# Kernel tuning notes

Measured on AMD Instinct MI355X. Metric: run time of the kernel, lower is better.

The kernel has to match this reference:

```python
import jax, jax.numpy as jnp
import numpy as np

CHUNK = 2048   # chunk_size from __init__
EPS = 1e-5     # BatchNorm eps (torch default)


def _proj(x, w, gamma, beta, mean, var):
    # 1x1 conv (no bias) + BatchNorm (eval, running stats) + ReLU
    y = jnp.einsum('bchw,oc->bohw', x, w)
    scale = gamma / jnp.sqrt(var + EPS)
    y = (y - mean[None, :, None, None]) * scale[None, :, None, None] + beta[None, :, None, None]
    return jax.nn.relu(y)


def setup_inputs() -> dict:
    key = jax.random.key(0)
    ks = jax.random.split(key, 8)
    B, Cl, Ci, Co, H, W = 2, 256, 512, 128, 128, 128
    return {
        'lidar_features': jax.random.normal(ks[0], (B, Cl, H, W), jnp.float32),
        'image_features': jax.random.normal(ks[1], (B, Ci, H, W), jnp.float32),
        # kaiming_normal fan_out for 1x1 conv: std = sqrt(2 / Co)
        'lidar_w': jax.random.normal(ks[2], (Co, Cl), jnp.float32) * np.sqrt(2.0 / Co),
        'lidar_gamma': jnp.ones((Co,), jnp.float32),
        'lidar_beta': jnp.zeros((Co,), jnp.float32),
        'lidar_mean': jax.random.normal(ks[3], (Co,), jnp.float32) * 0.1,
        'lidar_var': jax.random.uniform(ks[4], (Co,), jnp.float32, 0.5, 1.5),
        'image_w': jax.random.normal(ks[5], (Co, Ci), jnp.float32) * np.sqrt(2.0 / Co),
        'image_gamma': jnp.ones((Co,), jnp.float32),
        'image_beta': jnp.zeros((Co,), jnp.float32),
        'image_mean': jax.random.normal(ks[6], (Co,), jnp.float32) * 0.1,
        'image_var': jax.random.uniform(ks[7], (Co,), jnp.float32, 0.5, 1.5),
        'modality_weights': jnp.ones((2,), jnp.float32),
    }


def reference(lidar_features, image_features,
              lidar_w, lidar_gamma, lidar_beta, lidar_mean, lidar_var,
              image_w, image_gamma, image_beta, image_mean, image_var,
              modality_weights):
    lidar_proj = _proj(lidar_features, lidar_w, lidar_gamma, lidar_beta, lidar_mean, lidar_var)
    image_proj = _proj(image_features, image_w, image_gamma, image_beta, image_mean, image_var)
    # spatial sizes match by construction, so no interpolation branch
    B, C, H, W = lidar_proj.shape
    P = H * W
    n = P // CHUNK  # P chosen divisible by CHUNK
    # block-diagonal attention: q from image, k=v from lidar, per pixel chunk
    q = image_proj.reshape(B, C, P).transpose(0, 2, 1).reshape(B, n, CHUNK, C)
    k = lidar_proj.reshape(B, C, P).transpose(0, 2, 1).reshape(B, n, CHUNK, C)
    attn = jax.nn.softmax(jnp.einsum('bnqc,bnkc->bnqk', q, k) / jnp.sqrt(jnp.float32(C)), axis=-1)
    out = jnp.einsum('bnqk,bnkc->bnqc', attn, k)  # v == k (both are lidar_proj)
    fused = out.reshape(B, P, C).transpose(0, 2, 1).reshape(B, C, H, W)
    w = jax.nn.softmax(modality_weights)
    return w[0] * image_proj + w[1] * fused
```

## Files before the change

### kernel.cpp

```cpp
#include <hip/hip_runtime.h>
#include <hip/hip_bf16.h>

typedef __attribute__((ext_vector_type(4))) float f32x4;
typedef __attribute__((ext_vector_type(8))) short short8;

#define P_TOT 16384
#define NCO 128
#define EPS 1e-5f
#define ALPHA 0.12752269f

__device__ __forceinline__ unsigned short f2bf(float f) {
  union { float f; unsigned u; } v; v.f = f;
  unsigned r = v.u + 0x7FFFu + ((v.u >> 16) & 1u);
  return (unsigned short)(r >> 16);
}
__device__ __forceinline__ float bf2f(unsigned short h) {
  union { unsigned u; float f; } v; v.u = ((unsigned)h) << 16;
  return v.f;
}
__device__ __forceinline__ unsigned cvtpk_bf16(float lo, float hi) {
  unsigned r;
  asm("v_cvt_pk_bf16_f32 %0, %1, %2" : "=v"(r) : "v"(lo), "v"(hi));
  return r;
}
__device__ __forceinline__ void gload16(const void* g, void* l) {
  __builtin_amdgcn_global_load_lds(
      (const __attribute__((address_space(1))) unsigned*)g,
      (__attribute__((address_space(3))) unsigned*)l, 16, 0, 0);
}

__global__ __launch_bounds__(256) void proj_mfma(
    const float* __restrict__ Xl, const float* __restrict__ Xi,
    const float* __restrict__ Wl, const float* __restrict__ Wi,
    const float* __restrict__ lgm, const float* __restrict__ lbt,
    const float* __restrict__ lmn, const float* __restrict__ lvr,
    const float* __restrict__ igm, const float* __restrict__ ibt,
    const float* __restrict__ imn, const float* __restrict__ ivr,
    unsigned short* __restrict__ Lp, unsigned short* __restrict__ Ip,
    unsigned short* __restrict__ Vg)
{
  __shared__ __align__(16) char smem[36352];
  float* sc_l = (float*)(smem + 35328);
  float* sh_l = (float*)(smem + 35840);

  const int t = threadIdx.x;
  const int w = t >> 6, l = t & 63, l15 = l & 15, g = l >> 4;
  const int zz = blockIdx.y, b = zz & 1, mod = zz >> 1;
  const int pb = blockIdx.x * 128;

  const float* Xg = mod ? Xi : Xl;
  const float* Wg = mod ? Wi : Wl;
  const int Cin = mod ? 512 : 256;
  unsigned short* outp = mod ? Ip : Lp;

  if (t < 128) {
    const float* G = mod ? igm : lgm;
    const float* Bt = mod ? ibt : lbt;
    const float* M = mod ? imn : lmn;
    const float* V = mod ? ivr : lvr;
    float s = G[t] / sqrtf(V[t] + EPS);
    sc_l[t] = s;
    sh_l[t] = Bt[t] - M[t] * s;
  }

  f32x4 o[2][8];
#pragma unroll
  for (int qt = 0; qt < 2; ++qt)
#pragma unroll
    for (int nt = 0; nt < 8; ++nt) o[qt][nt] = (f32x4){0.f, 0.f, 0.f, 0.f};

  uint2 xr[8], wr[8];
  auto load_tiles = [&](int s) {
    int cc = s * 64;
#pragma unroll
    for (int i = 0; i < 8; ++i) {
      int e = t + 256 * i;
      int c = e >> 5, p4 = e & 31;
      f32x4 x = *(const f32x4*)(Xg + ((size_t)(b * Cin + cc + c)) * P_TOT + pb + p4 * 4);
      xr[i].x = cvtpk_bf16(x[0], x[1]);
      xr[i].y = cvtpk_bf16(x[2], x[3]);
    }
#pragma unroll
    for (int i = 0; i < 8; ++i) {
      int e = t + 256 * i;
      int co = e >> 4, c4 = e & 15;
      f32x4 wv = *(const f32x4*)(Wg + (size_t)co * Cin + cc + c4 * 4);
      wr[i].x = cvtpk_bf16(wv[0], wv[1]);
      wr[i].y = cvtpk_bf16(wv[2], wv[3]);
    }
  };

  load_tiles(0);
  const int nsteps = Cin >> 6;
  for (int s = 0; s < nsteps; ++s) {
    __syncthreads();
#pragma unroll
    for (int i = 0; i < 8; ++i) {
      int e = t + 256 * i;
      int c = e >> 5, p4 = e & 31;
      *(uint2*)(smem + c * 264 + p4 * 8) = xr[i];
    }
#pragma unroll
    for (int i = 0; i < 8; ++i) {
      int e = t + 256 * i;
      int co = e >> 4, c4 = e & 15;
      *(uint2*)(smem + 16896 + co * 144 + c4 * 8) = wr[i];
    }
    if (s + 1 < nsteps) load_tiles(s + 1);
    __syncthreads();

#pragma unroll
    for (int kkc = 0; kkc < 2; ++kkc) {
      short8 a[2];
#pragma unroll
      for (int qt = 0; qt < 2; ++qt) {
        const char* ab = smem + (kkc * 32 + g * 8) * 264 + (w * 32 + qt * 16 + l15) * 2;
        union { unsigned uu[4]; short8 v; } cv;
#pragma unroll
        for (int e2 = 0; e2 < 4; ++e2) {
          unsigned lo = *(const unsigned short*)(ab + (2 * e2) * 264);
          unsigned hi = *(const unsigned short*)(ab + (2 * e2 + 1) * 264);
          cv.uu[e2] = lo | (hi << 16);
        }
        a[qt] = cv.v;
      }
#pragma unroll
      for (int nt = 0; nt < 8; ++nt) {
        short8 wf = *(const short8*)(smem + 16896 + (nt * 16 + l15) * 144 + kkc * 64 + g * 16);
        o[0][nt] = __builtin_amdgcn_mfma_f32_16x16x32_bf16(a[0], wf, o[0][nt], 0, 0, 0);
        o[1][nt] = __builtin_amdgcn_mfma_f32_16x16x32_bf16(a[1], wf, o[1][nt], 0, 0, 0);
      }
    }
  }

  __syncthreads();
#pragma unroll
  for (int nt = 0; nt < 8; ++nt) {
    float scv = sc_l[nt * 16 + l15];
    float shv = sh_l[nt * 16 + l15];
#pragma unroll
    for (int qt = 0; qt < 2; ++qt)
#pragma unroll
      for (int r = 0; r < 4; ++r) {
        int p = w * 32 + qt * 16 + 4 * g + r;
        float y = fmaxf(fmaf(o[qt][nt][r], scv, shv), 0.f);
        *(unsigned short*)(smem + p * 272 + (nt * 16 + l15) * 2) = f2bf(y);
      }
  }
  __syncthreads();
  {
    int p = t >> 1, half = t & 1;
    const char* Tb = smem + p * 272 + half * 128;
    unsigned short* ob = outp + ((size_t)b * P_TOT + pb + p) * NCO + half * 64;
#pragma unroll
    for (int i = 0; i < 8; ++i)
      *(uint4*)(ob + i * 8) = *(const uint4*)(Tb + i * 16);
  }
  if (mod == 0) {
    int co = t & 127, ph = t >> 7;
    unsigned short* vb = Vg + ((size_t)b * NCO + co) * P_TOT + pb + ph * 64;
    unsigned pkv[32];
#pragma unroll
    for (int j2 = 0; j2 < 32; ++j2) {
      unsigned lo = *(const unsigned short*)(smem + (ph * 64 + 2 * j2) * 272 + co * 2);
      unsigned hi = *(const unsigned short*)(smem + (ph * 64 + 2 * j2 + 1) * 272 + co * 2);
      pkv[j2] = lo | (hi << 16);
    }
#pragma unroll
    for (int i = 0; i < 8; ++i)
      *(uint4*)(vb + i * 8) = *(const uint4*)&pkv[i * 4];
  }
}

__global__ __launch_bounds__(512) void attn_kernel(
    const unsigned short* __restrict__ Lp,
    const unsigned short* __restrict__ Ip,
    const unsigned short* __restrict__ Vg,
    const float* __restrict__ mw,
    float* __restrict__ out)
{
  __shared__ __align__(16) char smem[131072];

  const int t = threadIdx.x;
  const int half = t >> 8;
  const int t2 = t & 255;
  const int w = t2 >> 6, l = t & 63;
  const int l15 = l & 15, g = l >> 4;
  const int hb = half << 16;
  const int gid = blockIdx.x;
  const int bx = gid >> 4;
  const int chunk = gid & 7;
  const int b = (gid >> 3) & 1;
  const int pq0 = chunk * 2048 + bx * 128;
  const int qw = pq0 + w * 32;

  short8 qf[2][4];
#pragma unroll
  for (int qt = 0; qt < 2; ++qt)
#pragma unroll
    for (int kkc = 0; kkc < 4; ++kkc)
      qf[qt][kkc] = *(const short8*)(Ip +
          ((size_t)b * P_TOT + qw + qt * 16 + l15) * NCO + kkc * 32 + g * 8);

  const char* srcK[4];
  const char* srcV[4];
  int ldsOff[4];
#pragma unroll
  for (int i = 0; i < 4; ++i) {
    int pos = (w * 4 + i) * 4 + (l >> 4);
    int nt = pos >> 4, gp = (pos >> 2) & 3, rr = pos & 3;
    int kp = (nt >> 1) * 32 + gp * 8 + (nt & 1) * 4 + rr;
    srcK[i] = (const char*)Lp +
              ((size_t)b * P_TOT + chunk * 2048 + half * 1024 + kp) * 256 +
              (((l & 15) * 16) ^ ((pos & 7) << 4));
    int c = (w * 4 + i) * 8 + (l >> 3);
    srcV[i] = (const char*)Vg +
              (((size_t)(b * NCO + c)) * P_TOT + chunk * 2048 + half * 1024) * 2 +
              (((l & 7) * 16) ^ ((c & 7) << 4));
    ldsOff[i] = hb + (w * 4 + i) * 1024;
  }

  float m_[2] = {-1e30f, -1e30f}, lsum[2] = {0.f, 0.f};
  f32x4 o[2][8];
#pragma unroll
  for (int qt = 0; qt < 2; ++qt)
#pragma unroll
    for (int ct = 0; ct < 8; ++ct) o[qt][ct] = (f32x4){0.f, 0.f, 0.f, 0.f};

#pragma unroll
  for (int i = 0; i < 4; ++i) {
    gload16(srcK[i], smem + ldsOff[i]);
    gload16(srcV[i], smem + 32768 + ldsOff[i]);
  }
  __syncthreads();

  int cur = 0;
  for (int kt = 0; kt < 16; ++kt) {
    if (kt + 1 < 16) {
#pragma unroll
      for (int i = 0; i < 4; ++i) {
        gload16(srcK[i] + (size_t)(kt + 1) * 16384,
                smem + (cur ^ 1) * 16384 + ldsOff[i]);
        gload16(srcV[i] + (size_t)(kt + 1) * 128,
                smem + 32768 + (cur ^ 1) * 16384 + ldsOff[i]);
      }
    }
    const char* Kb = smem + hb + cur * 16384;
    const char* Vb = smem + hb + 32768 + cur * 16384;

    f32x4 s[2][4];
#pragma unroll
    for (int qt = 0; qt < 2; ++qt)
#pragma unroll
      for (int nt = 0; nt < 4; ++nt) s[qt][nt] = (f32x4){0.f, 0.f, 0.f, 0.f};
#pragma unroll
    for (int kkc = 0; kkc < 4; ++kkc) {
#pragma unroll
      for (int nt = 0; nt < 4; ++nt) {
        short8 kf = *(const short8*)(Kb + (nt * 16 + l15) * 256 +
                        ((kkc * 64 + g * 16) ^ ((l15 & 7) << 4)));
        s[0][nt] = __builtin_amdgcn_mfma_f32_16x16x32_bf16(kf, qf[0][kkc], s[0][nt], 0, 0, 0);
        s[1][nt] = __builtin_amdgcn_mfma_f32_16x16x32_bf16(kf, qf[1][kkc], s[1][nt], 0, 0, 0);
      }
    }

    unsigned pk[2][4][2];
    float f_[2];
    int upd[2];
#pragma unroll
    for (int qt = 0; qt < 2; ++qt) {
      float v0 = fmaxf(fmaxf(s[qt][0][0], s[qt][0][1]), fmaxf(s[qt][0][2], s[qt][0][3]));
      float v1 = fmaxf(fmaxf(s[qt][1][0], s[qt][1][1]), fmaxf(s[qt][1][2], s[qt][1][3]));
      float v2 = fmaxf(fmaxf(s[qt][2][0], s[qt][2][1]), fmaxf(s[qt][2][2], s[qt][2][3]));
      float v3 = fmaxf(fmaxf(s[qt][3][0], s[qt][3][1]), fmaxf(s[qt][3][2], s[qt][3][3]));
      float v = fmaxf(fmaxf(v0, v1), fmaxf(v2, v3));
      v = fmaxf(v, __shfl_xor(v, 16));
      v = fmaxf(v, __shfl_xor(v, 32));
      float pm = v * ALPHA;
      upd[qt] = __any(pm > m_[qt] + 8.f);
      float mn = m_[qt];
      if (upd[qt]) {
        mn = fmaxf(m_[qt], pm);
        f_[qt] = __builtin_amdgcn_exp2f(m_[qt] - mn);
        m_[qt] = mn;
      } else {
        f_[qt] = 1.f;
      }
      float ps = 0.f;
#pragma unroll
      for (int nt = 0; nt < 4; ++nt) {
#pragma unroll
        for (int r = 0; r < 4; ++r) {
          float p = __builtin_amdgcn_exp2f(s[qt][nt][r] * ALPHA - mn);
          s[qt][nt][r] = p;
          ps += p;
        }
        pk[qt][nt][0] = cvtpk_bf16(s[qt][nt][0], s[qt][nt][1]);
        pk[qt][nt][1] = cvtpk_bf16(s[qt][nt][2], s[qt][nt][3]);
      }
      ps += __shfl_xor(ps, 16);
      ps += __shfl_xor(ps, 32);
      lsum[qt] = lsum[qt] * f_[qt] + ps;
    }

#pragma unroll
    for (int qt = 0; qt < 2; ++qt)
      if (upd[qt]) {
#pragma unroll
        for (int r = 0; r < 4; ++r) {
          float fb = __shfl(f_[qt], 20 * g + r);
#pragma unroll
          for (int ct = 0; ct < 8; ++ct) o[qt][ct][r] *= fb;
        }
      }

#pragma unroll
    for (int kk2 = 0; kk2 < 2; ++kk2) {
      short8 af[2];
#pragma unroll
      for (int qt = 0; qt < 2; ++qt) {
        union { unsigned u[4]; short8 v; } x;
        x.u[0] = pk[qt][2 * kk2][0];
        x.u[1] = pk[qt][2 * kk2][1];
        x.u[2] = pk[qt][2 * kk2 + 1][0];
        x.u[3] = pk[qt][2 * kk2 + 1][1];
        af[qt] = x.v;
      }
#pragma unroll
      for (int ct = 0; ct < 8; ++ct) {
        short8 vf = *(const short8*)(Vb + (ct * 16 + l15) * 128 +
                        ((kk2 * 64 + g * 16) ^ ((l15 & 7) << 4)));
        o[0][ct] = __builtin_amdgcn_mfma_f32_16x16x32_bf16(af[0], vf, o[0][ct], 0, 0, 0);
        o[1][ct] = __builtin_amdgcn_mfma_f32_16x16x32_bf16(af[1], vf, o[1][ct], 0, 0, 0);
      }
    }
    __syncthreads();
    cur ^= 1;
  }

  float* Tp = (float*)smem;
  float* m1a = (float*)(smem + 67584);
  float* l1a = (float*)(smem + 68096);

  if (half == 1) {
#pragma unroll
    for (int qt = 0; qt < 2; ++qt) {
      int qb = w * 32 + qt * 16 + 4 * g;
#pragma unroll
      for (int ct = 0; ct < 8; ++ct) {
        int c = ct * 16 + l15;
        *(f32x4*)&Tp[c * 132 + qb] = o[qt][ct];
      }
      if (g == 0) {
        m1a[w * 32 + qt * 16 + l15] = m_[qt];
        l1a[w * 32 + qt * 16 + l15] = lsum[qt];
      }
    }
  }
  __syncthreads();

  float a0 = mw[0], a1 = mw[1];
  float mx = fmaxf(a0, a1);
  float e0 = __builtin_amdgcn_exp2f((a0 - mx) * 1.442695041f);
  float e1 = __builtin_amdgcn_exp2f((a1 - mx) * 1.442695041f);
  float w0m = e0 / (e0 + e1), w1m = e1 / (e0 + e1);

  if (half == 0) {
#pragma unroll
    for (int qt = 0; qt < 2; ++qt) {
      int qb = w * 32 + qt * 16 + 4 * g;
      f32x4 m1v = *(const f32x4*)&m1a[qb];
      f32x4 l1v = *(const f32x4*)&l1a[qb];
      float A[4], Bc[4];
#pragma unroll
      for (int r = 0; r < 4; ++r) {
        float m0r = __shfl(m_[qt], 20 * g + r);
        float l0r = __shfl(lsum[qt], 20 * g + r);
        float M = fmaxf(m0r, m1v[r]);
        float w0h = __builtin_amdgcn_exp2f(m0r - M);
        float w1h = __builtin_amdgcn_exp2f(m1v[r] - M);
        float L = w0h * l0r + w1h * l1v[r];
        A[r] = w1m * w0h / L;
        Bc[r] = w1m * w1h / L;
      }
#pragma unroll
      for (int ct = 0; ct < 8; ++ct) {
        int c = ct * 16 + l15;
        f32x4 o1 = *(const f32x4*)&Tp[c * 132 + qb];
#pragma unroll
        for (int r = 0; r < 4; ++r)
          o[qt][ct][r] = A[r] * o[qt][ct][r] + Bc[r] * o1[r];
      }
    }
  }
  __syncthreads();

  if (half == 0) {
#pragma unroll
    for (int qt = 0; qt < 2; ++qt) {
      int qb = w * 32 + qt * 16 + 4 * g;
#pragma unroll
      for (int ct = 0; ct < 8; ++ct) {
        int c = ct * 16 + l15;
        f32x4 v = o[qt][ct];
#pragma unroll
        for (int r = 0; r < 4; ++r) {
          float img = bf2f(Ip[((size_t)b * P_TOT + pq0 + qb + r) * NCO + c]);
          v[r] = w0m * img + v[r];
        }
        *(f32x4*)&Tp[c * 132 + qb] = v;
      }
    }
  }
  __syncthreads();
  {
    int cc = t >> 5;
    int q0 = (t & 31) * 4;
#pragma unroll
    for (int i2 = 0; i2 < 8; ++i2) {
      int c = cc + i2 * 16;
      float* Ob = out + ((size_t)b * NCO + c) * P_TOT + pq0 + q0;
      *(f32x4*)Ob = *(const f32x4*)&Tp[c * 132 + q0];
    }
  }
}

extern "C" void kernel_launch(void* const* d_in, const int* in_sizes, int n_in,
                              void* d_out, int out_size, void* d_ws, size_t ws_size,
                              hipStream_t stream) {
  const float* lidar = (const float*)d_in[0];
  const float* image = (const float*)d_in[1];
  const float* lw = (const float*)d_in[2];
  const float* lg = (const float*)d_in[3];
  const float* lb = (const float*)d_in[4];
  const float* lm = (const float*)d_in[5];
  const float* lv = (const float*)d_in[6];
  const float* iw = (const float*)d_in[7];
  const float* ig = (const float*)d_in[8];
  const float* ibt = (const float*)d_in[9];
  const float* im = (const float*)d_in[10];
  const float* iv = (const float*)d_in[11];
  const float* mw = (const float*)d_in[12];

  unsigned short* Lp = (unsigned short*)d_ws;
  unsigned short* Ip = Lp + (size_t)2 * P_TOT * NCO;
  unsigned short* Vg = Ip + (size_t)2 * P_TOT * NCO;

  dim3 gp(P_TOT / 128, 4);
  proj_mfma<<<gp, 256, 0, stream>>>(lidar, image, lw, iw,
                                    lg, lb, lm, lv, ig, ibt, im, iv,
                                    Lp, Ip, Vg);

  attn_kernel<<<dim3(256), 512, 0, stream>>>(Lp, Ip, Vg, mw, (float*)d_out);
}
```

Baseline: 81.33 us.

## Split attention into smaller blocks with 32-key tiles and MFMA priority hints

The attention kernel now runs 512 blocks of 256 threads instead of 256 blocks of 512, and each block handles 64 queries instead of 128. Each block uses two key-split groups with 32-key tiles over 32 iterations, halving LDS use to 64KB. The V tile layout and swizzle are reworked for the smaller tile. s_setprio is wrapped around the MFMA sections to favour matrix issue. The aim is more resident blocks per CU and better latency hiding, at the cost of more loop iterations, more barriers and K/V being reloaded by twice as many blocks.

New measurement: 123.8 us. 52.2% more time.

```diff
diff --git a/kernel.cpp b/kernel.cpp
--- a/kernel.cpp
+++ b/kernel.cpp
@@ -172,27 +172,26 @@
   }
 }
 
-__global__ __launch_bounds__(512) void attn_kernel(
+__global__ __launch_bounds__(256) void attn_kernel(
     const unsigned short* __restrict__ Lp,
     const unsigned short* __restrict__ Ip,
     const unsigned short* __restrict__ Vg,
     const float* __restrict__ mw,
     float* __restrict__ out)
 {
-  __shared__ __align__(16) char smem[131072];
+  __shared__ __align__(16) char smem[65536];
 
   const int t = threadIdx.x;
-  const int half = t >> 8;
-  const int t2 = t & 255;
-  const int w = t2 >> 6, l = t & 63;
+  const int w = t >> 6, l = t & 63;
+  const int qw = w & 1, kg = w >> 1;
   const int l15 = l & 15, g = l >> 4;
-  const int hb = half << 16;
+  const int kgb = kg << 15;
   const int gid = blockIdx.x;
-  const int bx = gid >> 4;
   const int chunk = gid & 7;
   const int b = (gid >> 3) & 1;
-  const int pq0 = chunk * 2048 + bx * 128;
-  const int qw = pq0 + w * 32;
+  const int bx = gid >> 4;
+  const int pq0 = chunk * 2048 + bx * 64;
+  const int qwb = pq0 + qw * 32;
 
   short8 qf[2][4];
 #pragma unroll
@@ -200,24 +199,27 @@
 #pragma unroll
     for (int kkc = 0; kkc < 4; ++kkc)
       qf[qt][kkc] = *(const short8*)(Ip +
-          ((size_t)b * P_TOT + qw + qt * 16 + l15) * NCO + kkc * 32 + g * 8);
+          ((size_t)b * P_TOT + qwb + qt * 16 + l15) * NCO + kkc * 32 + g * 8);
 
   const char* srcK[4];
   const char* srcV[4];
-  int ldsOff[4];
+  int ldsK[4], ldsV[4];
 #pragma unroll
   for (int i = 0; i < 4; ++i) {
-    int pos = (w * 4 + i) * 4 + (l >> 4);
-    int nt = pos >> 4, gp = (pos >> 2) & 3, rr = pos & 3;
-    int kp = (nt >> 1) * 32 + gp * 8 + (nt & 1) * 4 + rr;
+    int pos = qw * 16 + i * 4 + (l >> 4);
+    int kp = 8 * ((pos & 15) >> 2) + 4 * (pos >> 4) + (pos & 3);
     srcK[i] = (const char*)Lp +
-              ((size_t)b * P_TOT + chunk * 2048 + half * 1024 + kp) * 256 +
+              ((size_t)b * P_TOT + chunk * 2048 + kg * 1024 + kp) * 256 +
               (((l & 15) * 16) ^ ((pos & 7) << 4));
-    int c = (w * 4 + i) * 8 + (l >> 3);
+    ldsK[i] = kgb + (qw * 16 + i * 4) * 256;
+    int j = qw * 4 + i;
+    int pr = j * 8 + (l >> 3);
+    int logical = ((l & 7) * 16) ^ ((pr & 7) << 4);
+    int c = 2 * pr + (logical >> 6);
     srcV[i] = (const char*)Vg +
-              (((size_t)(b * NCO + c)) * P_TOT + chunk * 2048 + half * 1024) * 2 +
-              (((l & 7) * 16) ^ ((c & 7) << 4));
-    ldsOff[i] = hb + (w * 4 + i) * 1024;
+              ((size_t)(b * NCO + c) * P_TOT + chunk * 2048 + kg * 1024) * 2 +
+              (logical & 48);
+    ldsV[i] = kgb + 16384 + j * 1024;
   }
 
   float m_[2] = {-1e30f, -1e30f}, lsum[2] = {0.f, 0.f};
@@ -229,51 +231,51 @@
 
 #pragma unroll
   for (int i = 0; i < 4; ++i) {
-    gload16(srcK[i], smem + ldsOff[i]);
-    gload16(srcV[i], smem + 32768 + ldsOff[i]);
+    gload16(srcK[i], smem + ldsK[i]);
+    gload16(srcV[i], smem + ldsV[i]);
   }
   __syncthreads();
 
   int cur = 0;
-  for (int kt = 0; kt < 16; ++kt) {
-    if (kt + 1 < 16) {
+  for (int kt = 0; kt < 32; ++kt) {
+    if (kt + 1 < 32) {
 #pragma unroll
       for (int i = 0; i < 4; ++i) {
-        gload16(srcK[i] + (size_t)(kt + 1) * 16384,
-                smem + (cur ^ 1) * 16384 + ldsOff[i]);
-        gload16(srcV[i] + (size_t)(kt + 1) * 128,
-                smem + 32768 + (cur ^ 1) * 16384 + ldsOff[i]);
-      }
-    }
-    const char* Kb = smem + hb + cur * 16384;
-    const char* Vb = smem + hb + 32768 + cur * 16384;
-
-    f32x4 s[2][4];
+        gload16(srcK[i] + (size_t)(kt + 1) * 8192,
+                smem + ldsK[i] + (cur ^ 1) * 8192);
+        gload16(srcV[i] + (size_t)(kt + 1) * 64,
+                smem + ldsV[i] + (cur ^ 1) * 8192);
+      }
+    }
+    const char* Kb = smem + kgb + cur * 8192;
+    const char* Vb = smem + kgb + 16384 + cur * 8192;
+
+    f32x4 s[2][2];
 #pragma unroll
     for (int qt = 0; qt < 2; ++qt)
 #pragma unroll
-      for (int nt = 0; nt < 4; ++nt) s[qt][nt] = (f32x4){0.f, 0.f, 0.f, 0.f};
+      for (int nt = 0; nt < 2; ++nt) s[qt][nt] = (f32x4){0.f, 0.f, 0.f, 0.f};
+    __builtin_amdgcn_s_setprio(1);
 #pragma unroll
     for (int kkc = 0; kkc < 4; ++kkc) {
 #pragma unroll
-      for (int nt = 0; nt < 4; ++nt) {
+      for (int nt = 0; nt < 2; ++nt) {
         short8 kf = *(const short8*)(Kb + (nt * 16 + l15) * 256 +
                         ((kkc * 64 + g * 16) ^ ((l15 & 7) << 4)));
         s[0][nt] = __builtin_amdgcn_mfma_f32_16x16x32_bf16(kf, qf[0][kkc], s[0][nt], 0, 0, 0);
         s[1][nt] = __builtin_amdgcn_mfma_f32_16x16x32_bf16(kf, qf[1][kkc], s[1][nt], 0, 0, 0);
       }
     }
-
-    unsigned pk[2][4][2];
+    __builtin_amdgcn_s_setprio(0);
+
+    unsigned pk[2][4];
     float f_[2];
     int upd[2];
 #pragma unroll
     for (int qt = 0; qt < 2; ++qt) {
       float v0 = fmaxf(fmaxf(s[qt][0][0], s[qt][0][1]), fmaxf(s[qt][0][2], s[qt][0][3]));
       float v1 = fmaxf(fmaxf(s[qt][1][0], s[qt][1][1]), fmaxf(s[qt][1][2], s[qt][1][3]));
-      float v2 = fmaxf(fmaxf(s[qt][2][0], s[qt][2][1]), fmaxf(s[qt][2][2], s[qt][2][3]));
-      float v3 = fmaxf(fmaxf(s[qt][3][0], s[qt][3][1]), fmaxf(s[qt][3][2], s[qt][3][3]));
-      float v = fmaxf(fmaxf(v0, v1), fmaxf(v2, v3));
+      float v = fmaxf(v0, v1);
       v = fmaxf(v, __shfl_xor(v, 16));
       v = fmaxf(v, __shfl_xor(v, 32));
       float pm = v * ALPHA;
@@ -288,16 +290,17 @@
       }
       float ps = 0.f;
 #pragma unroll
-      for (int nt = 0; nt < 4; ++nt) {
+      for (int nt = 0; nt < 2; ++nt)
 #pragma unroll
         for (int r = 0; r < 4; ++r) {
           float p = __builtin_amdgcn_exp2f(s[qt][nt][r] * ALPHA - mn);
           s[qt][nt][r] = p;
           ps += p;
         }
-        pk[qt][nt][0] = cvtpk_bf16(s[qt][nt][0], s[qt][nt][1]);
-        pk[qt][nt][1] = cvtpk_bf16(s[qt][nt][2], s[qt][nt][3]);
-      }
+      pk[qt][0] = cvtpk_bf16(s[qt][0][0], s[qt][0][1]);
+      pk[qt][1] = cvtpk_bf16(s[qt][0][2], s[qt][0][3]);
+      pk[qt][2] = cvtpk_bf16(s[qt][1][0], s[qt][1][1]);
+      pk[qt][3] = cvtpk_bf16(s[qt][1][2], s[qt][1][3]);
       ps += __shfl_xor(ps, 16);
       ps += __shfl_xor(ps, 32);
       lsum[qt] = lsum[qt] * f_[qt] + ps;
@@ -314,46 +317,42 @@
         }
       }
 
-#pragma unroll
-    for (int kk2 = 0; kk2 < 2; ++kk2) {
-      short8 af[2];
-#pragma unroll
-      for (int qt = 0; qt < 2; ++qt) {
-        union { unsigned u[4]; short8 v; } x;
-        x.u[0] = pk[qt][2 * kk2][0];
-        x.u[1] = pk[qt][2 * kk2][1];
-        x.u[2] = pk[qt][2 * kk2 + 1][0];
-        x.u[3] = pk[qt][2 * kk2 + 1][1];
-        af[qt] = x.v;
-      }
-#pragma unroll
-      for (int ct = 0; ct < 8; ++ct) {
-        short8 vf = *(const short8*)(Vb + (ct * 16 + l15) * 128 +
-                        ((kk2 * 64 + g * 16) ^ ((l15 & 7) << 4)));
-        o[0][ct] = __builtin_amdgcn_mfma_f32_16x16x32_bf16(af[0], vf, o[0][ct], 0, 0, 0);
-        o[1][ct] = __builtin_amdgcn_mfma_f32_16x16x32_bf16(af[1], vf, o[1][ct], 0, 0, 0);
-      }
-    }
+    short8 af[2];
+#pragma unroll
+    for (int qt = 0; qt < 2; ++qt) {
+      union { unsigned u[4]; short8 v; } x;
+      x.u[0] = pk[qt][0]; x.u[1] = pk[qt][1];
+      x.u[2] = pk[qt][2]; x.u[3] = pk[qt][3];
+      af[qt] = x.v;
+    }
+    __builtin_amdgcn_s_setprio(1);
+#pragma unroll
+    for (int ct = 0; ct < 8; ++ct) {
+      int pr = ct * 8 + (l15 >> 1);
+      int phys = (((l15 & 1) * 64 + g * 16)) ^ ((pr & 7) << 4);
+      short8 vf = *(const short8*)(Vb + pr * 128 + phys);
+      o[0][ct] = __builtin_amdgcn_mfma_f32_16x16x32_bf16(af[0], vf, o[0][ct], 0, 0, 0);
+      o[1][ct] = __builtin_amdgcn_mfma_f32_16x16x32_bf16(af[1], vf, o[1][ct], 0, 0, 0);
+    }
+    __builtin_amdgcn_s_setprio(0);
     __syncthreads();
     cur ^= 1;
   }
 
   float* Tp = (float*)smem;
-  float* m1a = (float*)(smem + 67584);
-  float* l1a = (float*)(smem + 68096);
-
-  if (half == 1) {
+  float* m1a = (float*)(smem + 34816);
+  float* l1a = (float*)(smem + 35072);
+
+  if (kg == 1) {
 #pragma unroll
     for (int qt = 0; qt < 2; ++qt) {
-      int qb = w * 32 + qt * 16 + 4 * g;
-#pragma unroll
-      for (int ct = 0; ct < 8; ++ct) {
-        int c = ct * 16 + l15;
-        *(f32x4*)&Tp[c * 132 + qb] = o[qt][ct];
-      }
+      int qb = qw * 32 + qt * 16 + 4 * g;
+#pragma unroll
+      for (int ct = 0; ct < 8; ++ct)
+        *(f32x4*)&Tp[(ct * 16 + l15) * 68 + qb] = o[qt][ct];
       if (g == 0) {
-        m1a[w * 32 + qt * 16 + l15] = m_[qt];
-        l1a[w * 32 + qt * 16 + l15] = lsum[qt];
+        m1a[qw * 32 + qt * 16 + l15] = m_[qt];
+        l1a[qw * 32 + qt * 16 + l15] = lsum[qt];
       }
     }
   }
@@ -365,10 +364,10 @@
   float e1 = __builtin_amdgcn_exp2f((a1 - mx) * 1.442695041f);
   float w0m = e0 / (e0 + e1), w1m = e1 / (e0 + e1);
 
-  if (half == 0) {
+  if (kg == 0) {
 #pragma unroll
     for (int qt = 0; qt < 2; ++qt) {
-      int qb = w * 32 + qt * 16 + 4 * g;
+      int qb = qw * 32 + qt * 16 + 4 * g;
       f32x4 m1v = *(const f32x4*)&m1a[qb];
       f32x4 l1v = *(const f32x4*)&l1a[qb];
       float A[4], Bc[4];
@@ -386,7 +385,7 @@
 #pragma unroll
       for (int ct = 0; ct < 8; ++ct) {
         int c = ct * 16 + l15;
-        f32x4 o1 = *(const f32x4*)&Tp[c * 132 + qb];
+        f32x4 o1 = *(const f32x4*)&Tp[c * 68 + qb];
 #pragma unroll
         for (int r = 0; r < 4; ++r)
           o[qt][ct][r] = A[r] * o[qt][ct][r] + Bc[r] * o1[r];
@@ -395,10 +394,10 @@
   }
   __syncthreads();
 
-  if (half == 0) {
+  if (kg == 0) {
 #pragma unroll
     for (int qt = 0; qt < 2; ++qt) {
-      int qb = w * 32 + qt * 16 + 4 * g;
+      int qb = qw * 32 + qt * 16 + 4 * g;
 #pragma unroll
       for (int ct = 0; ct < 8; ++ct) {
         int c = ct * 16 + l15;
@@ -408,20 +407,17 @@
           float img = bf2f(Ip[((size_t)b * P_TOT + pq0 + qb + r) * NCO + c]);
           v[r] = w0m * img + v[r];
         }
-        *(f32x4*)&Tp[c * 132 + qb] = v;
+        *(f32x4*)&Tp[c * 68 + qb] = v;
       }
     }
   }
   __syncthreads();
   {
-    int cc = t >> 5;
-    int q0 = (t & 31) * 4;
-#pragma unroll
-    for (int i2 = 0; i2 < 8; ++i2) {
-      int c = cc + i2 * 16;
-      float* Ob = out + ((size_t)b * NCO + c) * P_TOT + pq0 + q0;
-      *(f32x4*)Ob = *(const f32x4*)&Tp[c * 132 + q0];
-    }
+    int c = t >> 1, qh = (t & 1) * 32;
+    float* Ob = out + ((size_t)b * NCO + c) * P_TOT + pq0 + qh;
+#pragma unroll
+    for (int i2 = 0; i2 < 8; ++i2)
+      *(f32x4*)(Ob + 4 * i2) = *(const f32x4*)&Tp[c * 68 + qh + 4 * i2];
   }
 }
 
@@ -451,5 +447,5 @@
                                     lg, lb, lm, lv, ig, ibt, im, iv,
                                     Lp, Ip, Vg);
 
-  attn_kernel<<<dim3(256), 512, 0, stream>>>(Lp, Ip, Vg, mw, (float*)d_out);
-}
+  attn_kernel<<<dim3(512), 256, 0, stream>>>(Lp, Ip, Vg, mw, (float*)d_out);
+}
```
